# Kernel tuning notes

Hardware: AMD Instinct MI355X
Metric: run time of the kernel (lower is better)

The kernel has to match this reference:

```python
import jax, jax.numpy as jnp
import numpy as np
from jax import lax


def _lstm(x, h0, c0, w_ih, w_hh, b_ih, b_hh):
    """PyTorch-convention LSTM (gate order i,f,g,o). x: [B,T,D] -> ys [B,T,H], hT, cT."""
    xg = jnp.einsum('btd,gd->btg', x, w_ih) + b_ih + b_hh  # input projection hoisted out of scan

    def step(carry, xt):
        h, c = carry
        g = xt + h @ w_hh.T
        i, f, gg, o = jnp.split(g, 4, axis=-1)
        c = jax.nn.sigmoid(f) * c + jax.nn.sigmoid(i) * jnp.tanh(gg)
        h = jax.nn.sigmoid(o) * jnp.tanh(c)
        return (h, c), h

    (hT, cT), ys = lax.scan(step, (h0, c0), jnp.swapaxes(xg, 0, 1))
    return jnp.swapaxes(ys, 0, 1), hT, cT


def setup_inputs() -> dict:
    B, T_ENC, T_DEC = 256, 256, 256
    E, H, ME = 128, 512, 16
    NT = 30000
    G = 4 * H
    ks = iter(jax.random.split(jax.random.key(0), 64))

    def nrm(shape, s=0.05):
        return jax.random.normal(next(ks), shape, jnp.float32) * s

    enc_in = E + E + 2 * ME  # t_emb + a_emb + meta = 288
    dec_in = E + E + 2 * ME  # t_emb + meta + prev_a_emb = 288

    def lstm_params(din):
        return nrm((G, din)), nrm((G, H)), nrm((G,)), nrm((G,))

    bif_w_ih, bif_w_hh, bif_b_ih, bif_b_hh = lstm_params(enc_in)
    bib_w_ih, bib_w_hh, bib_b_ih, bib_b_hh = lstm_params(enc_in)
    enc_w_ih, enc_w_hh, enc_b_ih, enc_b_hh = lstm_params(2 * H)
    dec_w_ih, dec_w_hh, dec_b_ih, dec_b_hh = lstm_params(dec_in)

    inp = dict(
        enc_q=jax.random.randint(next(ks), (B, T_ENC), 0, NT + 2),
        enc_a=jax.random.randint(next(ks), (B, T_ENC), 0, 2),
        enc_pos=jax.random.randint(next(ks), (B, T_ENC), 0, 22),
        enc_fmt=jax.random.randint(next(ks), (B, T_ENC), 0, 7),
        dec_q=jax.random.randint(next(ks), (B, T_DEC), 0, NT + 2),
        dec_a=jax.random.randint(next(ks), (B, T_DEC), 0, 2),
        dec_pos=jax.random.randint(next(ks), (B, T_DEC), 0, 22),
        dec_fmt=jax.random.randint(next(ks), (B, T_DEC), 0, 7),
        enc_last_a=jax.random.randint(next(ks), (B,), 0, 2),
        t_emb_w=nrm((NT + 2, E)).at[0].set(0.0),  # padding_idx=0
        a_emb_w=nrm((2, E)),
        pos_emb_w=nrm((22, ME)).at[0].set(0.0),
        fmt_emb_w=nrm((7, ME)).at[0].set(0.0),
        bif_w_ih=bif_w_ih, bif_w_hh=bif_w_hh, bif_b_ih=bif_b_ih, bif_b_hh=bif_b_hh,
        bib_w_ih=bib_w_ih, bib_w_hh=bib_w_hh, bib_b_ih=bib_b_ih, bib_b_hh=bib_b_hh,
        enc_w_ih=enc_w_ih, enc_w_hh=enc_w_hh, enc_b_ih=enc_b_ih, enc_b_hh=enc_b_hh,
        dec_w_ih=dec_w_ih, dec_w_hh=dec_w_hh, dec_b_ih=dec_b_ih, dec_b_hh=dec_b_hh,
        pred_w1=nrm((H, E + 2 * ME + H)), pred_b1=nrm((H,)),
        pred_w2=nrm((1, H)), pred_b2=nrm((1,)),
    )
    return inp


def reference(enc_q, enc_a, enc_pos, enc_fmt, dec_q, dec_a, dec_pos, dec_fmt, enc_last_a,
              t_emb_w, a_emb_w, pos_emb_w, fmt_emb_w,
              bif_w_ih, bif_w_hh, bif_b_ih, bif_b_hh,
              bib_w_ih, bib_w_hh, bib_b_ih, bib_b_hh,
              enc_w_ih, enc_w_hh, enc_b_ih, enc_b_hh,
              dec_w_ih, dec_w_hh, dec_b_ih, dec_b_hh,
              pred_w1, pred_b1, pred_w2, pred_b2):
    B = enc_q.shape[0]
    H = bif_w_hh.shape[1]
    h0 = jnp.zeros((B, H), jnp.float32)

    # ----- encode (full-length sequences; dropout = identity in eval) -----
    enc_x = jnp.concatenate([t_emb_w[enc_q], a_emb_w[enc_a],
                             pos_emb_w[enc_pos], fmt_emb_w[enc_fmt]], axis=-1)
    fwd_out, _, _ = _lstm(enc_x, h0, h0, bif_w_ih, bif_w_hh, bif_b_ih, bif_b_hh)
    bwd_out, _, _ = _lstm(enc_x[:, ::-1], h0, h0, bib_w_ih, bib_w_hh, bib_b_ih, bib_b_hh)
    bi_out = jnp.concatenate([fwd_out, bwd_out[:, ::-1]], axis=-1)  # [B,T,2H]
    _, hN, cN = _lstm(bi_out, h0, h0, enc_w_ih, enc_w_hh, enc_b_ih, enc_b_hh)

    # ----- decode (teacher forcing: prev answers = shifted dec_a) -----
    prev_a = jnp.concatenate([enc_last_a[:, None], dec_a[:, :-1]], axis=1)
    dec_t = t_emb_w[dec_q]                                            # [B,T,E]
    dec_m = jnp.concatenate([pos_emb_w[dec_pos], fmt_emb_w[dec_fmt]], axis=-1)
    dec_x = jnp.concatenate([dec_t, dec_m, a_emb_w[prev_a]], axis=-1)  # cat order as in decode()
    dec_out, _, _ = _lstm(dec_x, hN, cN, dec_w_ih, dec_w_hh, dec_b_ih, dec_b_hh)

    pred_in = jnp.concatenate([dec_t, dec_m, dec_out], axis=-1)       # [B,T,E+2*ME+H]
    hidden = jnp.tanh(pred_in @ pred_w1.T + pred_b1)
    logits = hidden @ pred_w2.T + pred_b2                              # [B,T,1]
    return jax.nn.sigmoid(logits[..., 0])                              # [B,T]
```

## Files before the change

### kernel.cpp

```cpp
#include <hip/hip_runtime.h>


using u16 = unsigned short;
using u32 = unsigned int;
using u64 = unsigned long long;
typedef float f32x4 __attribute__((ext_vector_type(4)));
typedef __bf16 bf16x8 __attribute__((ext_vector_type(8)));

__device__ __forceinline__ u16 f2bf(float f) {
  u32 u = __float_as_uint(f);
  u = (u + 0x7FFFu + ((u >> 16) & 1u)) >> 16;
  return (u16)u;
}
__device__ __forceinline__ float bf2f(u16 h) { return __uint_as_float(((u32)h) << 16); }
__device__ __forceinline__ float sigm(float x) { return 1.f / (1.f + __expf(-x)); }
__device__ __forceinline__ float tnh(float x) {
  float a = fabsf(x), e = __expf(-2.f * a);
  float t = (1.f - e) / (1.f + e);
  return x < 0.f ? -t : t;
}
__device__ __forceinline__ u64 ldA_u64(const u16* p) {
  return __hip_atomic_load((const u64*)p, __ATOMIC_RELAXED, __HIP_MEMORY_SCOPE_AGENT);
}
__device__ __forceinline__ void stA_u16(u16* p, u16 v) {
  __hip_atomic_store(p, v, __ATOMIC_RELAXED, __HIP_MEMORY_SCOPE_AGENT);
}
__device__ __forceinline__ void gload_lds16(const u16* g, u16* l) {
  __builtin_amdgcn_global_load_lds(
      (const __attribute__((address_space(1))) unsigned int*)g,
      (__attribute__((address_space(3))) unsigned int*)l, 16, 0, 0);
}

static const long SLOT_BI = 256L * 1024;
static const long SLOT_DO = 256L * 512;
static const long SLOT_XG = 256L * 2048;

template <int ACT, int KSTEPS, int PERM>
__device__ __forceinline__ void gemm_body(
    const u16* __restrict__ A1, long lda1, const u16* __restrict__ A2, long lda2, int ksplit,
    const u16* __restrict__ W, long ldw, const float* __restrict__ bias,
    u16* __restrict__ C, long ldc, int bx, int by, u16* sA, u16* sB) {
  const int tid = threadIdx.x;
  const int w = tid >> 6, lane = tid & 63;
  const int lr = lane & 15, lg = lane >> 4;
  const long mbase = (long)by * 128;
  const long nbase = (long)bx * 128;
  const int wm = (w >> 1) * 64, wn = (w & 1) * 64;
  const int s_r = lane >> 2, s_q = lane & 3;
  f32x4 acc[4][4] = {};
#pragma unroll 1
  for (int ks = 0; ks < KSTEPS; ks++) {
    const int kk = ks * 32;
    const u16* Asrc;
    long alda;
    int kofs;
    if (kk < ksplit) { Asrc = A1; alda = lda1; kofs = kk; }
    else             { Asrc = A2; alda = lda2; kofs = kk - ksplit; }
#pragma unroll
    for (int j = 0; j < 2; j++) {
      const int c = w * 2 + j;
      const long row = c * 16 + s_r;
      gload_lds16(Asrc + (mbase + row) * alda + kofs + s_q * 8, sA + c * 512);
      gload_lds16(W + (nbase + row) * ldw + kk + s_q * 8, sB + c * 512);
    }
    __syncthreads();
    bf16x8 a[4], b[4];
#pragma unroll
    for (int f = 0; f < 4; f++) {
      a[f] = *reinterpret_cast<const bf16x8*>(sA + (wm + f * 16 + lr) * 32 + lg * 8);
      b[f] = *reinterpret_cast<const bf16x8*>(sB + (wn + f * 16 + lr) * 32 + lg * 8);
    }
#pragma unroll
    for (int fm = 0; fm < 4; fm++)
#pragma unroll
      for (int fn = 0; fn < 4; fn++)
        acc[fm][fn] = __builtin_amdgcn_mfma_f32_16x16x32_bf16(a[fm], b[fn], acc[fm][fn], 0, 0, 0);
    __syncthreads();
  }
#pragma unroll
  for (int fm = 0; fm < 4; fm++)
#pragma unroll
    for (int fn = 0; fn < 4; fn++)
#pragma unroll
      for (int r = 0; r < 4; r++) {
        const long row = mbase + wm + fm * 16 + lg * 4 + r;
        const long col = nbase + wn + fn * 16 + lr;
        float v = acc[fm][fn][r] + bias[col];
        if (ACT == 1) v = tnh(v);
        const long cw = PERM ? (((col & 511) << 2) | (col >> 9)) : col;
        C[row * ldc + cw] = f2bf(v);
      }
}

template <int ACT, int KSTEPS, int PERM>
__global__ __launch_bounds__(256) void gemm_tile_k(
    const u16* __restrict__ A1, long lda1, const u16* __restrict__ A2, long lda2, int ksplit,
    const u16* __restrict__ W, long ldw, const float* __restrict__ bias,
    u16* __restrict__ C, long ldc) {
  __shared__ u16 sA[4096];
  __shared__ u16 sB[4096];
  gemm_body<ACT, KSTEPS, PERM>(A1, lda1, A2, lda2, ksplit, W, ldw, bias, C, ldc,
                               blockIdx.x, blockIdx.y, sA, sB);
}

struct XGJob2 {
  const u16 *Aa, *Ab, *Wa, *Wb;
  const float *ba, *bb;
  u16 *Xa, *Xb;
};
__global__ __launch_bounds__(256) void gemm_xg2_k(XGJob2 j) {
  __shared__ u16 sA[4096];
  __shared__ u16 sB[4096];
  if (blockIdx.z == 0)
    gemm_body<0, 9, 1>(j.Aa, 288, nullptr, 0, 1 << 30, j.Wa, 288, j.ba, j.Xa, 2048,
                       blockIdx.x, blockIdx.y, sA, sB);
  else
    gemm_body<0, 9, 1>(j.Ab, 288, nullptr, 0, 1 << 30, j.Wb, 288, j.bb, j.Xb, 2048,
                       blockIdx.x, blockIdx.y, sA, sB);
}

struct SeqP {
  const u16 *xgA, *xgB;
  const u16 *whA, *whB;
  float *cA, *cB;
  u16 *histA;
  u16 *h0, *h1;
  u32 *cnt;
  int k, CH;
};

template <int MODE>
__global__ __launch_bounds__(512, 2) void lstm_seq_k(SeqP p) {
  const int tid = threadIdx.x;
  const int w = tid >> 6, lane = tid & 63, lr = lane & 15, lg = lane >> 4;
  const int hct = w & 3, kh = w >> 2;
  int dir, rt, kb;
  if (MODE == 0) { dir = blockIdx.x >> 7; rt = (blockIdx.x >> 3) & 15; kb = blockIdx.x & 7; }
  else           { dir = 0;               rt = blockIdx.x >> 3;        kb = blockIdx.x & 7; }
  const u16* xg = (MODE == 0 && dir) ? p.xgB : p.xgA;
  const u16* wh = (MODE == 0 && dir) ? p.whB : p.whA;
  float* cbuf   = (MODE == 0 && dir) ? p.cB  : p.cA;
  const int rbase = rt * 16;
  const int hc0 = kb * 64 + hct * 16;
  const int kofs = kh * 256;
  u32* cnt = p.cnt + (long)((MODE == 0) ? (dir * 16 + rt) : rt) * 32;

  bf16x8 W[4][8];
#pragma unroll
  for (int g = 0; g < 4; g++)
#pragma unroll
    for (int ki = 0; ki < 8; ki++)
      W[g][ki] = *reinterpret_cast<const bf16x8*>(
          wh + (long)(g * 512 + hc0 + lr) * 512 + kofs + ki * 32 + lg * 8);

  const bool zero_init = (MODE <= 1) && (p.k == 0);
  float creg[4];
#pragma unroll
  for (int r = 0; r < 4; r++) {
    creg[r] = 0.f;
    if (kh == 0 && !zero_init)
      creg[r] = cbuf[(long)(rbase + lg * 4 + r) * 512 + hc0 + lr];
  }

  __shared__ f32x4 lacc[4][4][64];

  for (int ts = 0; ts < p.CH; ts++) {
    const int S = p.k * p.CH + ts;
    const u16* hp;
    u16* ho;
    long hstride;
    int slot;
    bool first;
    if (MODE == 0) {
      const int t = dir == 0 ? S : 255 - S;
      slot = dir == 0 ? ts : p.CH - 1 - ts;
      hstride = 1024;
      const int tp = dir == 0 ? t - 1 : t + 1;
      hp = p.histA + (long)tp * SLOT_BI + dir * 512;
      ho = p.histA + (long)t * SLOT_BI + dir * 512;
      first = (S == 0);
    } else if (MODE == 1) {
      slot = ts; hstride = 512;
      hp = (S & 1) ? p.h1 : p.h0;
      ho = (S & 1) ? p.h0 : p.h1;
      first = (S == 0);
    } else {
      slot = ts; hstride = 512;
      hp = (S == 0) ? p.h0 : p.histA + (long)(S - 1) * SLOT_DO;
      ho = p.histA + (long)S * SLOT_DO;
      first = false;
    }

    u64 xq[4];
    if (kh == 0) {
      const long xb2 = (long)slot * SLOT_XG;
      const int colh = hc0 + lr;
#pragma unroll
      for (int r = 0; r < 4; r++)
        xq[r] = *reinterpret_cast<const u64*>(
            xg + xb2 + (long)(rbase + lg * 4 + r) * 2048 + colh * 4);
    }

    f32x4 acc[4] = {};
    if (!first) {
      union AU { u64 q[2]; bf16x8 v; } au[8];
      const u16* abase = hp + (long)(rbase + lr) * hstride + kofs;
#pragma unroll
      for (int ki = 0; ki < 8; ki++) {
        au[ki].q[0] = ldA_u64(abase + ki * 32 + lg * 8);
        au[ki].q[1] = ldA_u64(abase + ki * 32 + lg * 8 + 4);
      }
#pragma unroll
      for (int ki = 0; ki < 8; ki++) {
#pragma unroll
        for (int g = 0; g < 4; g++)
          acc[g] = __builtin_amdgcn_mfma_f32_16x16x32_bf16(au[ki].v, W[g][ki], acc[g], 0, 0, 0);
      }
    }
    if (kh == 1) {
#pragma unroll
      for (int g = 0; g < 4; g++) lacc[hct][g][lane] = acc[g];
    }
    __syncthreads();
    if (kh == 0) {
#pragma unroll
      for (int g = 0; g < 4; g++) acc[g] += lacc[hct][g][lane];
#pragma unroll
      for (int r = 0; r < 4; r++) {
        const long row = rbase + lg * 4 + r;
        const int colh = hc0 + lr;
        float gi = acc[0][r] + bf2f((u16)(xq[r]));
        float gf = acc[1][r] + bf2f((u16)(xq[r] >> 16));
        float gg = acc[2][r] + bf2f((u16)(xq[r] >> 32));
        float go = acc[3][r] + bf2f((u16)(xq[r] >> 48));
        float cn = sigm(gf) * creg[r] + sigm(gi) * tnh(gg);
        creg[r] = cn;
        stA_u16(&ho[row * hstride + colh], f2bf(sigm(go) * tnh(cn)));
      }
    }
    __syncthreads();
    if (tid == 0) {
      __hip_atomic_fetch_add(cnt, 1u, __ATOMIC_RELAXED, __HIP_MEMORY_SCOPE_AGENT);
      if (ts != p.CH - 1) {
        const u32 tgt = 8u * (u32)(S + 1);
        while (__hip_atomic_load(cnt, __ATOMIC_RELAXED, __HIP_MEMORY_SCOPE_AGENT) < tgt)
          __builtin_amdgcn_s_sleep(1);
      }
    }
    __syncthreads();
  }
  if (kh == 0) {
#pragma unroll
    for (int r = 0; r < 4; r++)
      cbuf[(long)(rbase + lg * 4 + r) * 512 + hc0 + lr] = creg[r];
  }
}

struct WcvP {
  const float* s[9]; u16* d[9]; long n[9];
  const float *ba[4], *bb[4]; float* bd[4];
  u32* cnt;
};
__global__ __launch_bounds__(256) void initw_k(WcvP w) {
  const long g0 = (long)blockIdx.x * 256 + threadIdx.x;
  const long gs = (long)gridDim.x * 256;
  for (int seg = 0; seg < 9; seg++)
    for (long i = g0; i < w.n[seg]; i += gs) w.d[seg][i] = f2bf(w.s[seg][i]);
  for (int seg = 0; seg < 4; seg++)
    for (long i = g0; i < 2048; i += gs) w.bd[seg][i] = w.ba[seg][i] + w.bb[seg][i];
  for (long i = g0; i < 64 * 32; i += gs) w.cnt[i] = 0;
}

__global__ __launch_bounds__(256) void embed_k(
    const int* __restrict__ eq, const int* __restrict__ ea, const int* __restrict__ epos,
    const int* __restrict__ efmt, const int* __restrict__ dq, const int* __restrict__ da,
    const int* __restrict__ dpos, const int* __restrict__ dfmt, const int* __restrict__ last_a,
    const float* __restrict__ tw, const float* __restrict__ aw,
    const float* __restrict__ pw, const float* __restrict__ fw,
    u16* __restrict__ eout, u16* __restrict__ dout) {
  for (long row = blockIdx.x; row < 65536; row += gridDim.x) {
    const int t = (int)(row >> 8), b = (int)(row & 255);
    const long src = (long)b * 256 + t;
    {
      const int iq = eq[src], ia = ea[src], ip = epos[src], ifm = efmt[src];
      for (int col = threadIdx.x; col < 288; col += 256) {
        float v;
        if (col < 128)      v = tw[(long)iq * 128 + col];
        else if (col < 256) v = aw[(long)ia * 128 + (col - 128)];
        else if (col < 272) v = pw[(long)ip * 16 + (col - 256)];
        else                v = fw[(long)ifm * 16 + (col - 272)];
        eout[row * 288 + col] = f2bf(v);
      }
    }
    {
      const int iq = dq[src], ip = dpos[src], ifm = dfmt[src];
      const int pa = (t == 0) ? last_a[b] : da[src - 1];
      for (int col = threadIdx.x; col < 288; col += 256) {
        float v;
        if (col < 128)      v = tw[(long)iq * 128 + col];
        else if (col < 144) v = pw[(long)ip * 16 + (col - 128)];
        else if (col < 160) v = fw[(long)ifm * 16 + (col - 144)];
        else                v = aw[(long)pa * 128 + (col - 160)];
        dout[row * 288 + col] = f2bf(v);
      }
    }
  }
}

__global__ __launch_bounds__(256) void pred_out_k(
    const u16* __restrict__ hidden, const float* __restrict__ w2,
    const float* __restrict__ b2, float* __restrict__ out) {
  const int lane = threadIdx.x & 63;
  const float* wp = w2 + lane * 8;
  float wv[8];
#pragma unroll
  for (int j = 0; j < 8; j++) wv[j] = wp[j];
  const float bv = b2[0];
  for (long r = (long)blockIdx.x * 4 + (threadIdx.x >> 6); r < 65536; r += 8192) {
    const u16* hp = hidden + r * 512 + lane * 8;
    float s = 0.f;
#pragma unroll
    for (int j = 0; j < 8; j++) s += bf2f(hp[j]) * wv[j];
    for (int off = 32; off > 0; off >>= 1) s += __shfl_down(s, off);
    if (lane == 0) out[(r & 255) * 256 + (r >> 8)] = sigm(s + bv);
  }
}

extern "C" void kernel_launch(void* const* d_in, const int* in_sizes, int n_in,
                              void* d_out, int out_size, void* d_ws, size_t ws_size,
                              hipStream_t stream) {
  const int* enc_q     = (const int*)d_in[0];
  const int* enc_a     = (const int*)d_in[1];
  const int* enc_pos   = (const int*)d_in[2];
  const int* enc_fmt   = (const int*)d_in[3];
  const int* dec_q     = (const int*)d_in[4];
  const int* dec_a     = (const int*)d_in[5];
  const int* dec_pos   = (const int*)d_in[6];
  const int* dec_fmt   = (const int*)d_in[7];
  const int* enc_last  = (const int*)d_in[8];
  const float* t_emb   = (const float*)d_in[9];
  const float* a_emb   = (const float*)d_in[10];
  const float* pos_emb = (const float*)d_in[11];
  const float* fmt_emb = (const float*)d_in[12];
  const float* bif_w_ih = (const float*)d_in[13];
  const float* bif_w_hh = (const float*)d_in[14];
  const float* bif_b_ih = (const float*)d_in[15];
  const float* bif_b_hh = (const float*)d_in[16];
  const float* bib_w_ih = (const float*)d_in[17];
  const float* bib_w_hh = (const float*)d_in[18];
  const float* bib_b_ih = (const float*)d_in[19];
  const float* bib_b_hh = (const float*)d_in[20];
  const float* enc_w_ih = (const float*)d_in[21];
  const float* enc_w_hh = (const float*)d_in[22];
  const float* enc_b_ih = (const float*)d_in[23];
  const float* enc_b_hh = (const float*)d_in[24];
  const float* dec_w_ih = (const float*)d_in[25];
  const float* dec_w_hh = (const float*)d_in[26];
  const float* dec_b_ih = (const float*)d_in[27];
  const float* dec_b_hh = (const float*)d_in[28];
  const float* pred_w1 = (const float*)d_in[29];
  const float* pred_b1 = (const float*)d_in[30];
  const float* pred_w2 = (const float*)d_in[31];
  const float* pred_b2 = (const float*)d_in[32];
  (void)in_sizes; (void)n_in; (void)out_size;

  char* base = (char*)d_ws;
  size_t off = 0;
  auto alloc = [&](size_t bytes) -> char* {
    char* p = base + off;
    off = (off + bytes + 255) & ~(size_t)255;
    return p;
  };

  u16* wb_bif_ih = (u16*)alloc(2048L * 288 * 2);
  u16* wb_bib_ih = (u16*)alloc(2048L * 288 * 2);
  u16* wb_enc_ih = (u16*)alloc(2048L * 1024 * 2);
  u16* wb_dec_ih = (u16*)alloc(2048L * 288 * 2);
  u16* wb_bif_hh = (u16*)alloc(2048L * 512 * 2);
  u16* wb_bib_hh = (u16*)alloc(2048L * 512 * 2);
  u16* wb_enc_hh = (u16*)alloc(2048L * 512 * 2);
  u16* wb_dec_hh = (u16*)alloc(2048L * 512 * 2);
  u16* wb_pred1  = (u16*)alloc(512L * 672 * 2);
  float* bias_bif = (float*)alloc(2048 * 4);
  float* bias_bib = (float*)alloc(2048 * 4);
  float* bias_enc = (float*)alloc(2048 * 4);
  float* bias_dec = (float*)alloc(2048 * 4);
  float* c_bif = (float*)alloc(256L * 512 * 4);
  float* c_bib = (float*)alloc(256L * 512 * 4);
  float* c_enc = (float*)alloc(256L * 512 * 4);
  u16* h_enc0 = (u16*)alloc(256L * 512 * 2);
  u16* h_enc1 = (u16*)alloc(256L * 512 * 2);
  u32* cnt = (u32*)alloc(64L * 32 * 4);

  u16* bi    = (u16*)alloc(65536L * 1024 * 2);
  u16* dec_x = (u16*)alloc(65536L * 288 * 2);
  u16* enc_x = (u16*)alloc(65536L * 288 * 2);

  int CH = 128;
  while (CH > 8 && off + 2ull * CH * 256 * 2048 * 2 > ws_size) CH >>= 1;
  u16* X1 = (u16*)alloc((size_t)CH * 256 * 2048 * 2);
  u16* X2 = (u16*)alloc((size_t)CH * 256 * 2048 * 2);
  u16* decout = bi;
  u16* hidden = bi + 65536L * 512;
  const int NCH = 256 / CH;
  const int CHe = (CH * 2 <= 256) ? CH * 2 : 256;
  const int NCH2 = 256 / CHe;

  WcvP wc;
  wc.s[0] = bif_w_ih; wc.d[0] = wb_bif_ih; wc.n[0] = 2048L * 288;
  wc.s[1] = bib_w_ih; wc.d[1] = wb_bib_ih; wc.n[1] = 2048L * 288;
  wc.s[2] = enc_w_ih; wc.d[2] = wb_enc_ih; wc.n[2] = 2048L * 1024;
  wc.s[3] = dec_w_ih; wc.d[3] = wb_dec_ih; wc.n[3] = 2048L * 288;
  wc.s[4] = bif_w_hh; wc.d[4] = wb_bif_hh; wc.n[4] = 2048L * 512;
  wc.s[5] = bib_w_hh; wc.d[5] = wb_bib_hh; wc.n[5] = 2048L * 512;
  wc.s[6] = enc_w_hh; wc.d[6] = wb_enc_hh; wc.n[6] = 2048L * 512;
  wc.s[7] = dec_w_hh; wc.d[7] = wb_dec_hh; wc.n[7] = 2048L * 512;
  wc.s[8] = pred_w1;  wc.d[8] = wb_pred1;  wc.n[8] = 512L * 672;
  wc.ba[0] = bif_b_ih; wc.bb[0] = bif_b_hh; wc.bd[0] = bias_bif;
  wc.ba[1] = bib_b_ih; wc.bb[1] = bib_b_hh; wc.bd[1] = bias_bib;
  wc.ba[2] = enc_b_ih; wc.bb[2] = enc_b_hh; wc.bd[2] = bias_enc;
  wc.ba[3] = dec_b_ih; wc.bb[3] = dec_b_hh; wc.bd[3] = bias_dec;
  wc.cnt = cnt;
  initw_k<<<1024, 256, 0, stream>>>(wc);

  embed_k<<<2048, 256, 0, stream>>>(enc_q, enc_a, enc_pos, enc_fmt,
                                    dec_q, dec_a, dec_pos, dec_fmt, enc_last,
                                    t_emb, a_emb, pos_emb, fmt_emb, enc_x, dec_x);

  for (int k = 0; k < NCH; k++) {
    const int t0f = k * CH;
    const int t0b = 256 - (k + 1) * CH;
    XGJob2 j{enc_x + (long)t0f * 256 * 288, enc_x + (long)t0b * 256 * 288,
             wb_bif_ih, wb_bib_ih, bias_bif, bias_bib, X1, X2};
    gemm_xg2_k<<<dim3(16, CH * 2, 2), 256, 0, stream>>>(j);
    SeqP sp{X1, X2, wb_bif_hh, wb_bib_hh, c_bif, c_bib,
            bi, nullptr, nullptr, cnt, k, CH};
    lstm_seq_k<0><<<dim3(256), dim3(512), 0, stream>>>(sp);
  }

  for (int k = 0; k < NCH2; k++) {
    gemm_tile_k<0, 32, 1><<<dim3(16, CHe * 2), 256, 0, stream>>>(
        bi + (long)k * CHe * SLOT_BI, 1024, bi, 1024, 1024,
        wb_enc_ih, 1024, bias_enc, X1, 2048);
    SeqP sp{X1, nullptr, wb_enc_hh, nullptr, c_enc, nullptr,
            nullptr, h_enc0, h_enc1, cnt + 32L * 32, k, CHe};
    lstm_seq_k<1><<<dim3(128), dim3(512), 0, stream>>>(sp);
  }

  for (int k = 0; k < NCH2; k++) {
    gemm_tile_k<0, 9, 1><<<dim3(16, CHe * 2), 256, 0, stream>>>(
        dec_x + (long)k * CHe * 256 * 288, 288, dec_x, 288, 288,
        wb_dec_ih, 288, bias_dec, X1, 2048);
    SeqP sp{X1, nullptr, wb_dec_hh, nullptr, c_enc, nullptr,
            decout, h_enc0, nullptr, cnt + 48L * 32, k, CHe};
    lstm_seq_k<2><<<dim3(128), dim3(512), 0, stream>>>(sp);
  }

  gemm_tile_k<1, 21, 0><<<dim3(4, 512), 256, 0, stream>>>(
      dec_x, 288, decout, 512, 160, wb_pred1, 672, pred_b1, hidden, 512);
  pred_out_k<<<2048, 256, 0, stream>>>(hidden, pred_w2, pred_b2, (float*)d_out);
}
```

Before: 6.111 ms.

## Swizzle GEMM LDS layout and pre-permute input weights to drop scattered stores

Adds an XOR swizzle to how the GEMM tiles are written to and read from LDS, aiming to remove bank conflicts on the bf16x8 fragment reads. The gate-interleaving permutation that used to be applied per output element in the GEMM epilogue now happens once in weight init: W_ih rows and the combined biases are stored pre-permuted, so the epilogue writes contiguous columns. The non-permuted prediction GEMM still uses unpermuted pred_w1 and pred_b1 and stays correct. The cost is more complex index math in the init kernel and in the LDS addressing.

```diff
diff --git a/kernel.cpp b/kernel.cpp
--- a/kernel.cpp
+++ b/kernel.cpp
@@ -35,7 +35,7 @@
 static const long SLOT_DO = 256L * 512;
 static const long SLOT_XG = 256L * 2048;
 
-template <int ACT, int KSTEPS, int PERM>
+template <int ACT, int KSTEPS>
 __device__ __forceinline__ void gemm_body(
     const u16* __restrict__ A1, long lda1, const u16* __restrict__ A2, long lda2, int ksplit,
     const u16* __restrict__ W, long ldw, const float* __restrict__ bias,
@@ -47,6 +47,11 @@
   const long nbase = (long)bx * 128;
   const int wm = (w >> 1) * 64, wn = (w & 1) * 64;
   const int s_r = lane >> 2, s_q = lane & 3;
+  const int u_ = s_r >> 1;
+  const int sp = ((s_r & 1) << 2) | s_q;
+  const int s_log = sp ^ u_;
+  const int q_log = s_log & 3;
+  const int ric = u_ * 2 + (s_log >> 2);
   f32x4 acc[4][4] = {};
 #pragma unroll 1
   for (int ks = 0; ks < KSTEPS; ks++) {
@@ -59,16 +64,20 @@
 #pragma unroll
     for (int j = 0; j < 2; j++) {
       const int c = w * 2 + j;
-      const long row = c * 16 + s_r;
-      gload_lds16(Asrc + (mbase + row) * alda + kofs + s_q * 8, sA + c * 512);
-      gload_lds16(W + (nbase + row) * ldw + kk + s_q * 8, sB + c * 512);
+      const long row = c * 16 + ric;
+      gload_lds16(Asrc + (mbase + row) * alda + kofs + q_log * 8, sA + c * 512);
+      gload_lds16(W + (nbase + row) * ldw + kk + q_log * 8, sB + c * 512);
     }
     __syncthreads();
     bf16x8 a[4], b[4];
 #pragma unroll
     for (int f = 0; f < 4; f++) {
-      a[f] = *reinterpret_cast<const bf16x8*>(sA + (wm + f * 16 + lr) * 32 + lg * 8);
-      b[f] = *reinterpret_cast<const bf16x8*>(sB + (wn + f * 16 + lr) * 32 + lg * 8);
+      const int ra = wm + f * 16 + lr;
+      const int rb = wn + f * 16 + lr;
+      const int oa = (ra >> 1) * 64 + (((((ra & 1) << 2) | lg) ^ ((ra >> 1) & 7)) << 3);
+      const int ob = (rb >> 1) * 64 + (((((rb & 1) << 2) | lg) ^ ((rb >> 1) & 7)) << 3);
+      a[f] = *reinterpret_cast<const bf16x8*>(sA + oa);
+      b[f] = *reinterpret_cast<const bf16x8*>(sB + ob);
     }
 #pragma unroll
     for (int fm = 0; fm < 4; fm++)
@@ -87,20 +96,19 @@
         const long col = nbase + wn + fn * 16 + lr;
         float v = acc[fm][fn][r] + bias[col];
         if (ACT == 1) v = tnh(v);
-        const long cw = PERM ? (((col & 511) << 2) | (col >> 9)) : col;
-        C[row * ldc + cw] = f2bf(v);
-      }
-}
-
-template <int ACT, int KSTEPS, int PERM>
+        C[row * ldc + col] = f2bf(v);
+      }
+}
+
+template <int ACT, int KSTEPS>
 __global__ __launch_bounds__(256) void gemm_tile_k(
     const u16* __restrict__ A1, long lda1, const u16* __restrict__ A2, long lda2, int ksplit,
     const u16* __restrict__ W, long ldw, const float* __restrict__ bias,
     u16* __restrict__ C, long ldc) {
   __shared__ u16 sA[4096];
   __shared__ u16 sB[4096];
-  gemm_body<ACT, KSTEPS, PERM>(A1, lda1, A2, lda2, ksplit, W, ldw, bias, C, ldc,
-                               blockIdx.x, blockIdx.y, sA, sB);
+  gemm_body<ACT, KSTEPS>(A1, lda1, A2, lda2, ksplit, W, ldw, bias, C, ldc,
+                         blockIdx.x, blockIdx.y, sA, sB);
 }
 
 struct XGJob2 {
@@ -112,11 +120,11 @@
   __shared__ u16 sA[4096];
   __shared__ u16 sB[4096];
   if (blockIdx.z == 0)
-    gemm_body<0, 9, 1>(j.Aa, 288, nullptr, 0, 1 << 30, j.Wa, 288, j.ba, j.Xa, 2048,
-                       blockIdx.x, blockIdx.y, sA, sB);
+    gemm_body<0, 9>(j.Aa, 288, nullptr, 0, 1 << 30, j.Wa, 288, j.ba, j.Xa, 2048,
+                    blockIdx.x, blockIdx.y, sA, sB);
   else
-    gemm_body<0, 9, 1>(j.Ab, 288, nullptr, 0, 1 << 30, j.Wb, 288, j.bb, j.Xb, 2048,
-                       blockIdx.x, blockIdx.y, sA, sB);
+    gemm_body<0, 9>(j.Ab, 288, nullptr, 0, 1 << 30, j.Wb, 288, j.bb, j.Xb, 2048,
+                    blockIdx.x, blockIdx.y, sA, sB);
 }
 
 struct SeqP {
@@ -257,17 +265,30 @@
 }
 
 struct WcvP {
-  const float* s[9]; u16* d[9]; long n[9];
+  const float* s[9]; u16* d[9]; long n[9]; int permK[9];
   const float *ba[4], *bb[4]; float* bd[4];
   u32* cnt;
 };
 __global__ __launch_bounds__(256) void initw_k(WcvP w) {
   const long g0 = (long)blockIdx.x * 256 + threadIdx.x;
   const long gs = (long)gridDim.x * 256;
-  for (int seg = 0; seg < 9; seg++)
-    for (long i = g0; i < w.n[seg]; i += gs) w.d[seg][i] = f2bf(w.s[seg][i]);
+  for (int seg = 0; seg < 9; seg++) {
+    const int K = w.permK[seg];
+    if (K) {
+      for (long i = g0; i < w.n[seg]; i += gs) {
+        const long row = i / K, kk = i - row * K;
+        const long pr = ((row & 511) << 2) | (row >> 9);
+        w.d[seg][pr * K + kk] = f2bf(w.s[seg][i]);
+      }
+    } else {
+      for (long i = g0; i < w.n[seg]; i += gs) w.d[seg][i] = f2bf(w.s[seg][i]);
+    }
+  }
   for (int seg = 0; seg < 4; seg++)
-    for (long i = g0; i < 2048; i += gs) w.bd[seg][i] = w.ba[seg][i] + w.bb[seg][i];
+    for (long i = g0; i < 2048; i += gs) {
+      const long pi = ((i & 511) << 2) | (i >> 9);
+      w.bd[seg][pi] = w.ba[seg][i] + w.bb[seg][i];
+    }
   for (long i = g0; i < 64 * 32; i += gs) w.cnt[i] = 0;
 }
 
@@ -407,15 +428,15 @@
   const int NCH2 = 256 / CHe;
 
   WcvP wc;
-  wc.s[0] = bif_w_ih; wc.d[0] = wb_bif_ih; wc.n[0] = 2048L * 288;
-  wc.s[1] = bib_w_ih; wc.d[1] = wb_bib_ih; wc.n[1] = 2048L * 288;
-  wc.s[2] = enc_w_ih; wc.d[2] = wb_enc_ih; wc.n[2] = 2048L * 1024;
-  wc.s[3] = dec_w_ih; wc.d[3] = wb_dec_ih; wc.n[3] = 2048L * 288;
-  wc.s[4] = bif_w_hh; wc.d[4] = wb_bif_hh; wc.n[4] = 2048L * 512;
-  wc.s[5] = bib_w_hh; wc.d[5] = wb_bib_hh; wc.n[5] = 2048L * 512;
-  wc.s[6] = enc_w_hh; wc.d[6] = wb_enc_hh; wc.n[6] = 2048L * 512;
-  wc.s[7] = dec_w_hh; wc.d[7] = wb_dec_hh; wc.n[7] = 2048L * 512;
-  wc.s[8] = pred_w1;  wc.d[8] = wb_pred1;  wc.n[8] = 512L * 672;
+  wc.s[0] = bif_w_ih; wc.d[0] = wb_bif_ih; wc.n[0] = 2048L * 288;  wc.permK[0] = 288;
+  wc.s[1] = bib_w_ih; wc.d[1] = wb_bib_ih; wc.n[1] = 2048L * 288;  wc.permK[1] = 288;
+  wc.s[2] = enc_w_ih; wc.d[2] = wb_enc_ih; wc.n[2] = 2048L * 1024; wc.permK[2] = 1024;
+  wc.s[3] = dec_w_ih; wc.d[3] = wb_dec_ih; wc.n[3] = 2048L * 288;  wc.permK[3] = 288;
+  wc.s[4] = bif_w_hh; wc.d[4] = wb_bif_hh; wc.n[4] = 2048L * 512;  wc.permK[4] = 0;
+  wc.s[5] = bib_w_hh; wc.d[5] = wb_bib_hh; wc.n[5] = 2048L * 512;  wc.permK[5] = 0;
+  wc.s[6] = enc_w_hh; wc.d[6] = wb_enc_hh; wc.n[6] = 2048L * 512;  wc.permK[6] = 0;
+  wc.s[7] = dec_w_hh; wc.d[7] = wb_dec_hh; wc.n[7] = 2048L * 512;  wc.permK[7] = 0;
+  wc.s[8] = pred_w1;  wc.d[8] = wb_pred1;  wc.n[8] = 512L * 672;   wc.permK[8] = 0;
   wc.ba[0] = bif_b_ih; wc.bb[0] = bif_b_hh; wc.bd[0] = bias_bif;
   wc.ba[1] = bib_b_ih; wc.bb[1] = bib_b_hh; wc.bd[1] = bias_bib;
   wc.ba[2] = enc_b_ih; wc.bb[2] = enc_b_hh; wc.bd[2] = bias_enc;
@@ -439,7 +460,7 @@
   }
 
   for (int k = 0; k < NCH2; k++) {
-    gemm_tile_k<0, 32, 1><<<dim3(16, CHe * 2), 256, 0, stream>>>(
+    gemm_tile_k<0, 32><<<dim3(16, CHe * 2), 256, 0, stream>>>(
         bi + (long)k * CHe * SLOT_BI, 1024, bi, 1024, 1024,
         wb_enc_ih, 1024, bias_enc, X1, 2048);
     SeqP sp{X1, nullptr, wb_enc_hh, nullptr, c_enc, nullptr,
@@ -448,7 +469,7 @@
   }
 
   for (int k = 0; k < NCH2; k++) {
-    gemm_tile_k<0, 9, 1><<<dim3(16, CHe * 2), 256, 0, stream>>>(
+    gemm_tile_k<0, 9><<<dim3(16, CHe * 2), 256, 0, stream>>>(
         dec_x + (long)k * CHe * 256 * 288, 288, dec_x, 288, 288,
         wb_dec_ih, 288, bias_dec, X1, 2048);
     SeqP sp{X1, nullptr, wb_dec_hh, nullptr, c_enc, nullptr,
@@ -456,7 +477,7 @@
     lstm_seq_k<2><<<dim3(128), dim3(512), 0, stream>>>(sp);
   }
 
-  gemm_tile_k<1, 21, 0><<<dim3(4, 512), 256, 0, stream>>>(
+  gemm_tile_k<1, 21><<<dim3(4, 512), 256, 0, stream>>>(
       dec_x, 288, decout, 512, 160, wb_pred1, 672, pred_b1, hidden, 512);
   pred_out_k<<<2048, 256, 0, stream>>>(hidden, pred_w2, pred_b2, (float*)d_out);
 }
```

Result: faster. 5.822 ms, median of 3 (-4.7%).
